# Kernel optimization log

Measured on AMD Instinct MI355X. Metric: run time of the kernel, lower is better.

## Reference

```python
import jax, jax.numpy as jnp
import numpy as np

N_NODES = 50000
N_EDGES = 800000
DIM = 128
LN_EPS = 1e-5


def setup_inputs() -> dict:
    key = jax.random.key(0)
    k1, k2, k3, k4 = jax.random.split(key, 4)
    h = jax.random.normal(k1, (N_NODES, DIM), dtype=jnp.float32)
    edge_index = jax.random.randint(k2, (2, N_EDGES), 0, N_NODES, dtype=jnp.int64)
    W = jax.random.normal(k3, (DIM, DIM), dtype=jnp.float32) / np.sqrt(DIM)
    b = jnp.zeros((DIM,), dtype=jnp.float32)
    gamma = jnp.ones((DIM,), dtype=jnp.float32)
    beta = jnp.zeros((DIM,), dtype=jnp.float32)
    t = jnp.zeros((), dtype=jnp.float32)
    return {"t": t, "h": h, "edge_index": edge_index, "batch_size": N_NODES,
            "W": W, "b": b, "gamma": gamma, "beta": beta}


def _gcn_conv(h, edge_index, W, b):
    """PyG-style GCNConv: D^{-1/2} (A+I) D^{-1/2} (h W) + b."""
    N = h.shape[0]
    loops = jnp.arange(N, dtype=edge_index.dtype)
    src = jnp.concatenate([edge_index[0], loops])  # [E+N]
    dst = jnp.concatenate([edge_index[1], loops])  # [E+N]
    # degree (with self loops) on destination nodes
    deg = jax.ops.segment_sum(jnp.ones_like(dst, dtype=h.dtype), dst, num_segments=N)
    dinv = jnp.where(deg > 0, jax.lax.rsqrt(deg), 0.0)
    norm = dinv[src] * dinv[dst]                    # [E+N]
    xw = h @ W                                      # [N, D]
    msg = xw[src] * norm[:, None]                   # gather + scale, [E+N, D]
    agg = jax.ops.segment_sum(msg, dst, num_segments=N)  # scatter-add, [N, D]
    return agg + b


def reference(t, h, edge_index, batch_size, W, b, gamma, beta):
    if h.ndim == 1:
        h = h[None, :]
    dh = _gcn_conv(h, edge_index, W, b)
    # LayerNorm over feature dim, then tanh
    mean = jnp.mean(dh, axis=-1, keepdims=True)
    var = jnp.mean(jnp.square(dh - mean), axis=-1, keepdims=True)
    dh = (dh - mean) * jax.lax.rsqrt(var + LN_EPS) * gamma + beta
    dh = jnp.tanh(dh)
    return (dh, jnp.zeros_like(edge_index), jnp.zeros_like(jnp.asarray(batch_size)))
```

## Files before the change

kernel.cpp:

```cpp
#include <hip/hip_runtime.h>
#include <math.h>

#define NN 50000
#define NE 800000
#define D  128
#define CNT_BLOCKS 3125
#define GEMM_BLOCKS 782

typedef __attribute__((ext_vector_type(8))) short bf16x8;
typedef __attribute__((ext_vector_type(4))) float f32x4;

__device__ __forceinline__ unsigned short f32_to_bf16(float f) {
    unsigned u = __float_as_uint(f);
    u = u + 0x7FFFu + ((u >> 16) & 1u);
    return (unsigned short)(u >> 16);
}

__device__ __forceinline__ float fast_tanh(float x) {
    float e = __expf(2.0f * x);
    return fmaf(-2.0f, __builtin_amdgcn_rcpf(e + 1.0f), 1.0f);
}

#define GLD16(P, VO, BASE)                                              \
    asm volatile(                                                       \
        "global_load_dword %0, %16, %32\n\t"                            \
        "global_load_dword %1, %17, %32\n\t"                            \
        "global_load_dword %2, %18, %32\n\t"                            \
        "global_load_dword %3, %19, %32\n\t"                            \
        "global_load_dword %4, %20, %32\n\t"                            \
        "global_load_dword %5, %21, %32\n\t"                            \
        "global_load_dword %6, %22, %32\n\t"                            \
        "global_load_dword %7, %23, %32\n\t"                            \
        "global_load_dword %8, %24, %32\n\t"                            \
        "global_load_dword %9, %25, %32\n\t"                            \
        "global_load_dword %10, %26, %32\n\t"                           \
        "global_load_dword %11, %27, %32\n\t"                           \
        "global_load_dword %12, %28, %32\n\t"                           \
        "global_load_dword %13, %29, %32\n\t"                           \
        "global_load_dword %14, %30, %32\n\t"                           \
        "global_load_dword %15, %31, %32\n\t"                           \
        "s_waitcnt vmcnt(0)"                                            \
        : "=&v"(P[0]),  "=&v"(P[1]),  "=&v"(P[2]),  "=&v"(P[3]),        \
          "=&v"(P[4]),  "=&v"(P[5]),  "=&v"(P[6]),  "=&v"(P[7]),        \
          "=&v"(P[8]),  "=&v"(P[9]),  "=&v"(P[10]), "=&v"(P[11]),       \
          "=&v"(P[12]), "=&v"(P[13]), "=&v"(P[14]), "=&v"(P[15])        \
        : "v"(VO[0]),  "v"(VO[1]),  "v"(VO[2]),  "v"(VO[3]),            \
          "v"(VO[4]),  "v"(VO[5]),  "v"(VO[6]),  "v"(VO[7]),            \
          "v"(VO[8]),  "v"(VO[9]),  "v"(VO[10]), "v"(VO[11]),           \
          "v"(VO[12]), "v"(VO[13]), "v"(VO[14]), "v"(VO[15]),           \
          "s"(BASE))

__global__ __launch_bounds__(256) void k_init(
        const float* __restrict__ Wg, int* __restrict__ deg,
        unsigned short* __restrict__ wpk, unsigned short* __restrict__ zb) {
    int tid = threadIdx.x;
    int idx = blockIdx.x * 256 + tid;

    if (idx < NN / 4) ((int4*)deg)[idx] = (int4){0, 0, 0, 0};

    if (blockIdx.x == 0) {
#pragma unroll 8
        for (int i = 0; i < 64; i++) {
            int o = i * 256 + tid;
            int j = o & 7, frag = o >> 3;
            int lo = frag & 15, quad = (frag >> 4) & 3;
            int kt = (frag >> 6) & 3, nt = frag >> 8;
            wpk[o] = f32_to_bf16(Wg[(kt * 32 + quad * 8 + j) * 128 + nt * 16 + lo]);
        }
    }
    if (blockIdx.x == 1 && tid < 64)
        ((unsigned*)(zb + (size_t)NN * D))[tid] = 0u;
}

__global__ __launch_bounds__(256) void k_count(
        const int* __restrict__ ei, int* __restrict__ deg,
        int* __restrict__ ell, int* __restrict__ outtail, int tailN) {
    int g = blockIdx.x * 256 + threadIdx.x;

    {
        int tail4 = tailN >> 2;
        for (int i = g; i < tail4; i += CNT_BLOCKS * 256)
            ((int4*)outtail)[i] = (int4){0, 0, 0, 0};
        if (g == 0)
            for (int k2 = tail4 << 2; k2 < tailN; k2++) outtail[k2] = 0;
    }

    int s = ei[g];
    int d = ei[NE + g];
    int r = atomicAdd(&deg[d], 1);
    if (r < 64) ell[(size_t)d * 64 + r] = s;
}

__global__ __launch_bounds__(256) void k_gemm_scale(
        const float* __restrict__ h, const uint4* __restrict__ wpk4,
        const int* __restrict__ deg, unsigned short* __restrict__ zb) {
    int tid = threadIdx.x;
    int gid = blockIdx.x;
    int w = tid >> 6, lane = tid & 63;
    int quad = lane >> 4, lo = lane & 15;
    int rowBase = gid * 64 + w * 16;
    int rowA = rowBase + lo; if (rowA > NN - 1) rowA = NN - 1;
    const float4* h4 = (const float4*)h;

    bf16x8 af[4];
#pragma unroll
    for (int kt = 0; kt < 4; kt++) {
        float4 u = h4[(size_t)rowA * 32 + kt * 8 + quad * 2];
        float4 v = h4[(size_t)rowA * 32 + kt * 8 + quad * 2 + 1];
        bf16x8 a;
        a[0] = (short)f32_to_bf16(u.x); a[1] = (short)f32_to_bf16(u.y);
        a[2] = (short)f32_to_bf16(u.z); a[3] = (short)f32_to_bf16(u.w);
        a[4] = (short)f32_to_bf16(v.x); a[5] = (short)f32_to_bf16(v.y);
        a[6] = (short)f32_to_bf16(v.z); a[7] = (short)f32_to_bf16(v.w);
        af[kt] = a;
    }

    f32x4 acc[8];
#pragma unroll
    for (int nt = 0; nt < 8; nt++) acc[nt] = (f32x4){0.f, 0.f, 0.f, 0.f};

#pragma unroll
    for (int kt = 0; kt < 4; kt++)
#pragma unroll
        for (int nt = 0; nt < 8; nt++) {
            uint4 tb = wpk4[nt * 256 + kt * 64 + lane];
            acc[nt] = __builtin_amdgcn_mfma_f32_16x16x32_bf16(
                af[kt], __builtin_bit_cast(bf16x8, tb), acc[nt], 0, 0, 0);
        }

#pragma unroll
    for (int reg = 0; reg < 4; reg++) {
        int row = rowBase + quad * 4 + reg;
        if (row < NN) {
            float dn = rsqrtf((float)deg[row] + 1.0f);
#pragma unroll
            for (int nt = 0; nt < 8; nt++)
                zb[(size_t)row * D + nt * 16 + lo] = f32_to_bf16(acc[nt][reg] * dn);
        }
    }
}

__global__ __launch_bounds__(256) void k_gather_ln(
        const int* __restrict__ deg, const int* __restrict__ ell,
        const unsigned* __restrict__ zbu,
        const float* __restrict__ bias, const float* __restrict__ gamma,
        const float* __restrict__ beta, float* __restrict__ out) {
    int tid = threadIdx.x;
    int w = tid >> 6, lane = tid & 63;
    int rowBase = blockIdx.x * 16 + w * 4;
    unsigned lane4 = (unsigned)(lane << 2);

    int m0[4]; float dn[4]; unsigned selfz[4]; int v[4];
#pragma unroll
    for (int r = 0; r < 4; r++) {
        int row = rowBase + r;
        int dg = __builtin_amdgcn_readfirstlane(deg[row]);
        dn[r] = rsqrtf((float)dg + 1.0f);
        m0[r] = (dg > 64) ? 64 : dg;
        selfz[r] = zbu[(size_t)row * 64 + lane];
        int t0 = ell[(size_t)row * 64 + lane];
        v[r] = (lane < m0[r]) ? t0 : NN;
    }

    float ax[4], ay[4];
#pragma unroll
    for (int r = 0; r < 4; r++) {
        ax[r] = __uint_as_float(selfz[r] << 16);
        ay[r] = __uint_as_float(selfz[r] & 0xFFFF0000u);
    }

    float2 x[4];
#pragma unroll
    for (int r = 0; r < 4; r++) {
        int nb = (m0[r] + 15) >> 4;
        for (int jb = 0; jb < nb; ++jb) {
            int j = jb << 4;
            unsigned vo[16], p[16];
#pragma unroll
            for (int q = 0; q < 16; q++) {
                int sq = __builtin_amdgcn_readlane(v[r], j + q);
                vo[q] = ((unsigned)sq << 8) + lane4;
            }
            GLD16(p, vo, zbu);
#pragma unroll
            for (int q = 0; q < 16; q++) {
                ax[r] += __uint_as_float(p[q] << 16);
                ay[r] += __uint_as_float(p[q] & 0xFFFF0000u);
            }
        }
        x[r].x = ax[r] * dn[r];
        x[r].y = ay[r] * dn[r];
    }

    float2 bi = ((const float2*)bias)[lane];
    float2 ga = ((const float2*)gamma)[lane];
    float2 be = ((const float2*)beta)[lane];
#pragma unroll
    for (int r = 0; r < 4; r++) {
        int row = rowBase + r;
        float y0 = x[r].x + bi.x;
        float y1 = x[r].y + bi.y;
        float s = y0 + y1;
#pragma unroll
        for (int off = 32; off > 0; off >>= 1) s += __shfl_xor(s, off, 64);
        float m = s * (1.0f / 128.0f);
        float v0f = y0 - m, v1f = y1 - m;
        float vs = v0f * v0f + v1f * v1f;
#pragma unroll
        for (int off = 32; off > 0; off >>= 1) vs += __shfl_xor(vs, off, 64);
        float rstd = rsqrtf(vs * (1.0f / 128.0f) + 1e-5f);
        float2 o;
        o.x = fast_tanh(v0f * rstd * ga.x + be.x);
        o.y = fast_tanh(v1f * rstd * ga.y + be.y);
        *(float2*)&out[(size_t)row * D + lane * 2] = o;
    }
}

extern "C" void kernel_launch(void* const* d_in, const int* in_sizes, int n_in,
                              void* d_out, int out_size, void* d_ws, size_t ws_size,
                              hipStream_t stream) {
    const float* h     = (const float*)d_in[1];
    const int*   ei    = (const int*)  d_in[2];
    const float* Wg    = (const float*)d_in[4];
    const float* b     = (const float*)d_in[5];
    const float* gamma = (const float*)d_in[6];
    const float* beta  = (const float*)d_in[7];
    float* out = (float*)d_out;

    char* wsb = (char*)d_ws;
    unsigned short* wpk = (unsigned short*)(wsb);
    int*            deg = (int*)(wsb + 32768);
    int*            ell = (int*)(wsb + 232768);
    unsigned short* zb  = (unsigned short*)(wsb + 13032768);

    int tailN = out_size - NN * D;
    int* outtail = (int*)(out + (size_t)NN * D);

    k_init       <<<64,          256, 0, stream>>>(Wg, deg, wpk, zb);
    k_count      <<<CNT_BLOCKS,  256, 0, stream>>>(ei, deg, ell, outtail, tailN);
    k_gemm_scale <<<GEMM_BLOCKS, 256, 0, stream>>>(h, (const uint4*)wpk, deg, zb);
    k_gather_ln  <<<NN / 16,     256, 0, stream>>>(deg, ell, (const unsigned*)zb, b, gamma, beta, out);
}
```

Measured before the change: 188.5 us.

## Fuse degree counting with GEMM and move source normalization into gather

Merges the edge-count/ELL-build kernel and the bf16 GEMM into one launch, with odd blocks doing atomics and even blocks doing MFMA, so the two independent stages overlap and one launch is removed. Because the GEMM no longer waits on degrees, the per-source D^-1/2 scaling moves into the gather kernel, which now loads each neighbour's degree alongside its feature row and computes an rsqrt per edge. Edge processing is also vectorized to four edges per thread. The cost is extra degree loads and rsqrt work in the gather loop, plus a sentinel degree entry for padded neighbours.

Measured after the change: 180.5 us. -4.3%, faster.

```diff
diff --git a/kernel.cpp b/kernel.cpp
--- a/kernel.cpp
+++ b/kernel.cpp
@@ -4,8 +4,7 @@
 #define NN 50000
 #define NE 800000
 #define D  128
-#define CNT_BLOCKS 3125
-#define GEMM_BLOCKS 782
+#define NROLES 1564
 
 typedef __attribute__((ext_vector_type(8))) short bf16x8;
 typedef __attribute__((ext_vector_type(4))) float f32x4;
@@ -20,6 +19,34 @@
     float e = __expf(2.0f * x);
     return fmaf(-2.0f, __builtin_amdgcn_rcpf(e + 1.0f), 1.0f);
 }
+
+#define GLD16_NOWAIT(P, VO, BASE)                                       \
+    asm volatile(                                                       \
+        "global_load_dword %0, %16, %32\n\t"                            \
+        "global_load_dword %1, %17, %32\n\t"                            \
+        "global_load_dword %2, %18, %32\n\t"                            \
+        "global_load_dword %3, %19, %32\n\t"                            \
+        "global_load_dword %4, %20, %32\n\t"                            \
+        "global_load_dword %5, %21, %32\n\t"                            \
+        "global_load_dword %6, %22, %32\n\t"                            \
+        "global_load_dword %7, %23, %32\n\t"                            \
+        "global_load_dword %8, %24, %32\n\t"                            \
+        "global_load_dword %9, %25, %32\n\t"                            \
+        "global_load_dword %10, %26, %32\n\t"                           \
+        "global_load_dword %11, %27, %32\n\t"                           \
+        "global_load_dword %12, %28, %32\n\t"                           \
+        "global_load_dword %13, %29, %32\n\t"                           \
+        "global_load_dword %14, %30, %32\n\t"                           \
+        "global_load_dword %15, %31, %32"                               \
+        : "=&v"(P[0]),  "=&v"(P[1]),  "=&v"(P[2]),  "=&v"(P[3]),        \
+          "=&v"(P[4]),  "=&v"(P[5]),  "=&v"(P[6]),  "=&v"(P[7]),        \
+          "=&v"(P[8]),  "=&v"(P[9]),  "=&v"(P[10]), "=&v"(P[11]),       \
+          "=&v"(P[12]), "=&v"(P[13]), "=&v"(P[14]), "=&v"(P[15])        \
+        : "v"(VO[0]),  "v"(VO[1]),  "v"(VO[2]),  "v"(VO[3]),            \
+          "v"(VO[4]),  "v"(VO[5]),  "v"(VO[6]),  "v"(VO[7]),            \
+          "v"(VO[8]),  "v"(VO[9]),  "v"(VO[10]), "v"(VO[11]),           \
+          "v"(VO[12]), "v"(VO[13]), "v"(VO[14]), "v"(VO[15]),           \
+          "s"(BASE))
 
 #define GLD16(P, VO, BASE)                                              \
     asm volatile(                                                       \
@@ -57,6 +84,7 @@
     int idx = blockIdx.x * 256 + tid;
 
     if (idx < NN / 4) ((int4*)deg)[idx] = (int4){0, 0, 0, 0};
+    if (idx == NN / 4) deg[NN] = 0;
 
     if (blockIdx.x == 0) {
 #pragma unroll 8
@@ -72,30 +100,41 @@
         ((unsigned*)(zb + (size_t)NN * D))[tid] = 0u;
 }
 
-__global__ __launch_bounds__(256) void k_count(
+__global__ __launch_bounds__(256) void k_count_gemm(
+        const float* __restrict__ h, const uint4* __restrict__ wpk4,
         const int* __restrict__ ei, int* __restrict__ deg,
-        int* __restrict__ ell, int* __restrict__ outtail, int tailN) {
-    int g = blockIdx.x * 256 + threadIdx.x;
+        int* __restrict__ ell, unsigned short* __restrict__ zb,
+        int* __restrict__ outtail, int tailN) {
+    int tid = threadIdx.x;
+    int bid = blockIdx.x;
 
     {
+        int gt = bid * 256 + tid;
         int tail4 = tailN >> 2;
-        for (int i = g; i < tail4; i += CNT_BLOCKS * 256)
+        for (int i = gt; i < tail4; i += NROLES * 256)
             ((int4*)outtail)[i] = (int4){0, 0, 0, 0};
-        if (g == 0)
+        if (gt == 0)
             for (int k2 = tail4 << 2; k2 < tailN; k2++) outtail[k2] = 0;
     }
 
-    int s = ei[g];
-    int d = ei[NE + g];
-    int r = atomicAdd(&deg[d], 1);
-    if (r < 64) ell[(size_t)d * 64 + r] = s;
-}
-
-__global__ __launch_bounds__(256) void k_gemm_scale(
-        const float* __restrict__ h, const uint4* __restrict__ wpk4,
-        const int* __restrict__ deg, unsigned short* __restrict__ zb) {
-    int tid = threadIdx.x;
-    int gid = blockIdx.x;
+    if (bid & 1) {
+        int g = (bid >> 1) * 256 + tid;
+        if (g < NE / 4) {
+            int4 s4 = ((const int4*)ei)[g];
+            int4 d4 = ((const int4*)(ei + NE))[g];
+            int r0 = atomicAdd(&deg[d4.x], 1);
+            int r1 = atomicAdd(&deg[d4.y], 1);
+            int r2 = atomicAdd(&deg[d4.z], 1);
+            int r3 = atomicAdd(&deg[d4.w], 1);
+            if (r0 < 64) ell[(size_t)d4.x * 64 + r0] = s4.x;
+            if (r1 < 64) ell[(size_t)d4.y * 64 + r1] = s4.y;
+            if (r2 < 64) ell[(size_t)d4.z * 64 + r2] = s4.z;
+            if (r3 < 64) ell[(size_t)d4.w * 64 + r3] = s4.w;
+        }
+        return;
+    }
+
+    int gid = bid >> 1;
     int w = tid >> 6, lane = tid & 63;
     int quad = lane >> 4, lo = lane & 15;
     int rowBase = gid * 64 + w * 16;
@@ -132,10 +171,9 @@
     for (int reg = 0; reg < 4; reg++) {
         int row = rowBase + quad * 4 + reg;
         if (row < NN) {
-            float dn = rsqrtf((float)deg[row] + 1.0f);
 #pragma unroll
             for (int nt = 0; nt < 8; nt++)
-                zb[(size_t)row * D + nt * 16 + lo] = f32_to_bf16(acc[nt][reg] * dn);
+                zb[(size_t)row * D + nt * 16 + lo] = f32_to_bf16(acc[nt][reg]);
         }
     }
 }
@@ -165,8 +203,8 @@
     float ax[4], ay[4];
 #pragma unroll
     for (int r = 0; r < 4; r++) {
-        ax[r] = __uint_as_float(selfz[r] << 16);
-        ay[r] = __uint_as_float(selfz[r] & 0xFFFF0000u);
+        ax[r] = dn[r] * __uint_as_float(selfz[r] << 16);
+        ay[r] = dn[r] * __uint_as_float(selfz[r] & 0xFFFF0000u);
     }
 
     float2 x[4];
@@ -175,17 +213,23 @@
         int nb = (m0[r] + 15) >> 4;
         for (int jb = 0; jb < nb; ++jb) {
             int j = jb << 4;
-            unsigned vo[16], p[16];
+            unsigned vo[16], vod[16], dgq[16], p[16];
 #pragma unroll
             for (int q = 0; q < 16; q++) {
                 int sq = __builtin_amdgcn_readlane(v[r], j + q);
-                vo[q] = ((unsigned)sq << 8) + lane4;
+                vo[q]  = ((unsigned)sq << 8) + lane4;
+                vod[q] = (unsigned)sq << 2;
             }
+            GLD16_NOWAIT(dgq, vod, deg);
             GLD16(p, vo, zbu);
+            float dnq[16];
+#pragma unroll
+            for (int q = 0; q < 16; q++)
+                dnq[q] = rsqrtf((float)(int)dgq[q] + 1.0f);
 #pragma unroll
             for (int q = 0; q < 16; q++) {
-                ax[r] += __uint_as_float(p[q] << 16);
-                ay[r] += __uint_as_float(p[q] & 0xFFFF0000u);
+                ax[r] = fmaf(dnq[q], __uint_as_float(p[q] << 16), ax[r]);
+                ay[r] = fmaf(dnq[q], __uint_as_float(p[q] & 0xFFFF0000u), ay[r]);
             }
         }
         x[r].x = ax[r] * dn[r];
@@ -230,14 +274,13 @@
     char* wsb = (char*)d_ws;
     unsigned short* wpk = (unsigned short*)(wsb);
     int*            deg = (int*)(wsb + 32768);
-    int*            ell = (int*)(wsb + 232768);
-    unsigned short* zb  = (unsigned short*)(wsb + 13032768);
+    int*            ell = (int*)(wsb + 237568);
+    unsigned short* zb  = (unsigned short*)(wsb + 13037568);
 
     int tailN = out_size - NN * D;
     int* outtail = (int*)(out + (size_t)NN * D);
 
-    k_init       <<<64,          256, 0, stream>>>(Wg, deg, wpk, zb);
-    k_count      <<<CNT_BLOCKS,  256, 0, stream>>>(ei, deg, ell, outtail, tailN);
-    k_gemm_scale <<<GEMM_BLOCKS, 256, 0, stream>>>(h, (const uint4*)wpk, deg, zb);
-    k_gather_ln  <<<NN / 16,     256, 0, stream>>>(deg, ell, (const unsigned*)zb, b, gamma, beta, out);
-}
+    k_init       <<<64,      256, 0, stream>>>(Wg, deg, wpk, zb);
+    k_count_gemm <<<NROLES,  256, 0, stream>>>(h, (const uint4*)wpk, ei, deg, ell, zb, outtail, tailN);
+    k_gather_ln  <<<NN / 16, 256, 0, stream>>>(deg, ell, (const unsigned*)zb, b, gamma, beta, out);
+}
```
